# Performance work log

Hardware: AMD Instinct MI355X
Metric: run time of the kernel (lower is better)

The kernel has to match this reference:

```python
import jax, jax.numpy as jnp
import numpy as np

B, P, O, C = 64, 8732, 32, 81
IMG = 224.0
THRESH = 0.5
NEG_POS = 3.0
ALPHA = 1.0


def cxcy_to_xy(b):
    return jnp.concatenate([b[..., :2] - b[..., 2:] / 2, b[..., :2] + b[..., 2:] / 2], -1)


def xy_to_cxcy(b):
    return jnp.concatenate([(b[..., :2] + b[..., 2:]) / 2, b[..., 2:] - b[..., :2]], -1)


def coco_to_xy(b):  # [x, y, w, h] -> [xmin, ymin, xmax, ymax]
    return jnp.concatenate([b[..., :2], b[..., :2] + b[..., 2:]], -1)


def cxcy_to_gcxgcy(cxcy, priors):  # SSD offset encoding, variances 10 / 5
    g_cxcy = (cxcy[..., :2] - priors[..., :2]) / (priors[..., 2:] / 10.0)
    g_wh = jnp.log(cxcy[..., 2:] / priors[..., 2:]) * 5.0
    return jnp.concatenate([g_cxcy, g_wh], -1)


def pairwise_iou(a, b):  # a: [O,4] xy, b: [P,4] xy -> [O,P]
    lt = jnp.maximum(a[:, None, :2], b[None, :, :2])
    rb = jnp.minimum(a[:, None, 2:], b[None, :, 2:])
    wh = jnp.clip(rb - lt, 0.0)
    inter = wh[..., 0] * wh[..., 1]
    area_a = (a[:, 2] - a[:, 0]) * (a[:, 3] - a[:, 1])
    area_b = (b[:, 2] - b[:, 0]) * (b[:, 3] - b[:, 1])
    return inter / (area_a[:, None] + area_b[None, :] - inter)


def setup_inputs() -> dict:
    key = jax.random.key(0)
    k1, k2, k3, k4, k5, k6, k7 = jax.random.split(key, 7)
    pred_locs = jax.random.normal(k1, (B, P, 4), dtype=jnp.float32)
    pred_scores = jax.random.normal(k2, (B, P, C), dtype=jnp.float32)
    # COCO-format gt boxes [x, y, w, h] in pixel coords, guaranteed inside image
    xy = jax.random.uniform(k3, (B, O, 2), minval=0.0, maxval=IMG * 0.55)
    wh = jax.random.uniform(k4, (B, O, 2), minval=8.0, maxval=IMG * 0.4)
    gt_boxes = jnp.concatenate([xy, wh], -1)
    gt_labels = jax.random.randint(k5, (B, O), 1, C)  # foreground labels 1..C-1
    p_cxcy = jax.random.uniform(k6, (P, 2), minval=0.05, maxval=0.95)
    p_wh = jax.random.uniform(k7, (P, 2), minval=0.05, maxval=0.5)
    priors_cxcy = jnp.concatenate([p_cxcy, p_wh], -1)
    return {"pred_locs": pred_locs, "pred_scores": pred_scores,
            "gt_boxes": gt_boxes, "gt_labels": gt_labels,
            "priors_cxcy": priors_cxcy}


def reference(pred_locs, pred_scores, gt_boxes, gt_labels, priors_cxcy):
    priors_xy = cxcy_to_xy(priors_cxcy)

    def match(boxes_coco, labels):  # one image: [O,4] coco, [O] int
        boxes_xy = coco_to_xy(boxes_coco) / IMG  # normalize to [0,1]
        ov = pairwise_iou(boxes_xy, priors_xy)  # [O, P]
        overlap_for_prior = ov.max(axis=0)       # [P]
        object_for_prior = ov.argmax(axis=0)     # [P]
        prior_for_object = ov.argmax(axis=1)     # [O]
        # force each object to claim its best prior
        object_for_prior = object_for_prior.at[prior_for_object].set(jnp.arange(O))
        overlap_for_prior = overlap_for_prior.at[prior_for_object].set(1.0)
        label_for_prior = labels[object_for_prior]
        label_for_prior = jnp.where(overlap_for_prior < THRESH, 0, label_for_prior)
        true_locs = cxcy_to_gcxgcy(xy_to_cxcy(boxes_xy[object_for_prior]), priors_cxcy)
        return true_locs, label_for_prior

    true_locs, true_classes = jax.vmap(match)(gt_boxes, gt_labels)  # [B,P,4], [B,P]

    positive = true_classes != 0          # [B, P]
    n_pos = positive.sum(axis=1)          # [B]
    n_pos_cl = jnp.maximum(n_pos, 1).astype(jnp.float32)
    n_hard_neg = NEG_POS * n_pos_cl

    # SmoothL1 (beta=1), mean over positive prior coords
    diff = jnp.abs(pred_locs - true_locs)
    sl1 = jnp.where(diff < 1.0, 0.5 * diff * diff, diff - 0.5)  # [B,P,4]
    total_pos = n_pos.sum()
    loc_loss = jnp.where(
        total_pos > 0,
        jnp.where(positive[..., None], sl1, 0.0).sum()
        / jnp.maximum(total_pos * 4, 1).astype(jnp.float32),
        0.0,
    )

    # per-prior cross entropy
    logp = jax.nn.log_softmax(pred_scores, axis=-1)
    ce = -jnp.take_along_axis(logp, true_classes[..., None], axis=-1)[..., 0]  # [B,P]

    conf_pos_sum = jnp.where(positive, ce, 0.0).sum()
    ce_neg = jnp.where(positive, 0.0, ce)
    ce_neg_sorted = -jnp.sort(-ce_neg, axis=1)  # descending per image
    ranks = jnp.arange(P)[None, :]
    hard = ranks < n_hard_neg[:, None]
    conf_hard_neg_sum = jnp.where(hard, ce_neg_sorted, 0.0).sum()

    conf_loss = (conf_hard_neg_sum + conf_pos_sum) / n_pos_cl.sum()
    return conf_loss + ALPHA * loc_loss
```

## Files before the change

kernel.cpp:

```cpp
#include <hip/hip_runtime.h>
#include <cstdint>
#include <cstddef>

#define BB 64
#define PP 8732
#define OO 32
#define CC 81
#define NBM 35
#define NB2 273

__global__ __launch_bounds__(256) void k_match(
    const float* __restrict__ gt_boxes,
    const float4* __restrict__ priors,
    float* __restrict__ ovl, int* __restrict__ obj,
    unsigned long long* __restrict__ part)
{
    int b = blockIdx.y, blk = blockIdx.x;
    int tid = threadIdx.x;
    int p = blk * 256 + tid;
    bool pv = p < PP;
    __shared__ float bx1[OO], by1[OO], bx2[OO], by2[OO], bar[OO];
    __shared__ float mat[OO][264];
    __shared__ unsigned long long po[OO][8];
    if (tid < OO) {
        const float* g = gt_boxes + ((size_t)b * OO + tid) * 4;
        float x1 = g[0] / 224.0f, y1 = g[1] / 224.0f;
        float x2 = (g[0] + g[2]) / 224.0f, y2 = (g[1] + g[3]) / 224.0f;
        bx1[tid] = x1; by1[tid] = y1; bx2[tid] = x2; by2[tid] = y2;
        bar[tid] = (x2 - x1) * (y2 - y1);
    }
    __syncthreads();
    float4 pr = priors[pv ? p : 0];
    float px1 = pr.x - pr.z * 0.5f, py1 = pr.y - pr.w * 0.5f;
    float px2 = pr.x + pr.z * 0.5f, py2 = pr.y + pr.w * 0.5f;
    float parea = (px2 - px1) * (py2 - py1);
    float best = -1.0f; int bo = 0;
    #pragma unroll
    for (int o = 0; o < OO; ++o) {
        float lx = fmaxf(bx1[o], px1), ly = fmaxf(by1[o], py1);
        float rx = fminf(bx2[o], px2), ry = fminf(by2[o], py2);
        float w = fmaxf(rx - lx, 0.0f), h = fmaxf(ry - ly, 0.0f);
        float inter = w * h;
        float iou = inter / (bar[o] + parea - inter);
        iou = pv ? iou : 0.0f;
        mat[o][tid] = iou;
        if (iou > best) { best = iou; bo = o; }
    }
    if (pv) {
        size_t idx = (size_t)b * PP + p;
        ovl[idx] = best;
        obj[idx] = bo;
    }
    __syncthreads();
    {
        int o = tid >> 3, j = tid & 7;
        float bv = -1.0f; int bt = 0;
        #pragma unroll
        for (int k = 0; k < 32; ++k) {
            int t = j + 8 * k;
            float v = mat[o][t];
            if (v > bv) { bv = v; bt = t; }
        }
        unsigned pg = (unsigned)(blk * 256 + bt);
        po[o][j] = ((unsigned long long)__float_as_uint(bv) << 32)
                 | (unsigned long long)(0xFFFFFFFFu - pg);
    }
    __syncthreads();
    if (tid < OO) {
        unsigned long long m = po[tid][0];
        #pragma unroll
        for (int j = 1; j < 8; ++j) if (po[tid][j] > m) m = po[tid][j];
        part[((size_t)b * NBM + blk) * OO + tid] = m;
    }
}

__global__ void k_force(const unsigned long long* __restrict__ part,
                        float* __restrict__ ovl, int* __restrict__ obj)
{
    int b = blockIdx.x;
    __shared__ int s_pfo[OO];
    int t = threadIdx.x;
    if (t < OO) {
        unsigned long long m = part[((size_t)b * NBM + 0) * OO + t];
        for (int blk = 1; blk < NBM; ++blk) {
            unsigned long long v = part[((size_t)b * NBM + blk) * OO + t];
            if (v > m) m = v;
        }
        s_pfo[t] = (int)(0xFFFFFFFFu - (unsigned)(m & 0xFFFFFFFFull));
    }
    __syncthreads();
    if (t == 0) {
        for (int o = 0; o < OO; ++o) {
            int p = s_pfo[o];
            obj[(size_t)b * PP + p] = o;
            ovl[(size_t)b * PP + p] = 1.0f;
        }
    }
}

__global__ __launch_bounds__(256) void k_ce(
    const float* __restrict__ scores,
    const float4* __restrict__ pred_locs,
    const float* __restrict__ gt_boxes,
    const int* __restrict__ gt_labels,
    const float4* __restrict__ priors,
    const float* __restrict__ ovl, const int* __restrict__ obj,
    float* __restrict__ ceneg,
    float* __restrict__ pp_posce, float* __restrict__ pp_sl1,
    int* __restrict__ pp_np)
{
    int b = blockIdx.y;
    int group = threadIdx.x >> 4, lane = threadIdx.x & 15;
    int p0 = blockIdx.x * 32 + group;
    int p1 = p0 + 16;
    bool v0 = p0 < PP, v1 = p1 < PP;
    size_t i0 = (size_t)b * PP + (size_t)(v0 ? p0 : 0);
    size_t i1 = (size_t)b * PP + (size_t)(v1 ? p1 : 0);
    __shared__ float s_posce, s_sl1;
    __shared__ int s_np;
    if (threadIdx.x == 0) { s_posce = 0.f; s_sl1 = 0.f; s_np = 0; }
    __syncthreads();
    int lab0 = 0, ob0 = 0, lab1 = 0, ob1 = 0;
    if (v0) { float ov = ovl[i0]; ob0 = obj[i0]; lab0 = (ov < 0.5f) ? 0 : gt_labels[b * OO + ob0]; }
    if (v1) { float ov = ovl[i1]; ob1 = obj[i1]; lab1 = (ov < 0.5f) ? 0 : gt_labels[b * OO + ob1]; }
    const float* r0 = scores + i0 * CC;
    const float* r1 = scores + i1 * CC;
    float a0[6], a1[6];
    #pragma unroll
    for (int k = 0; k < 6; ++k) {
        int c = lane + 16 * k;
        bool cv = c < CC;
        a0[k] = (v0 && cv) ? r0[c] : -INFINITY;
        a1[k] = (v1 && cv) ? r1[c] : -INFINITY;
    }
    float se0 = 0.f, xl0 = 0.f, se1 = 0.f, xl1 = 0.f;
    #pragma unroll
    for (int k = 0; k < 6; ++k) {
        int c = lane + 16 * k;
        if (c < CC) {
            se0 += __expf(a0[k]); if (c == lab0) xl0 = a0[k];
            se1 += __expf(a1[k]); if (c == lab1) xl1 = a1[k];
        }
    }
    #pragma unroll
    for (int s = 8; s >= 1; s >>= 1) {
        se0 += __shfl_xor(se0, s, 16);
        xl0 += __shfl_xor(xl0, s, 16);
        se1 += __shfl_xor(se1, s, 16);
        xl1 += __shfl_xor(xl1, s, 16);
    }
    if (lane == 0) {
        #pragma unroll
        for (int pass = 0; pass < 2; ++pass) {
            bool vv = pass ? v1 : v0;
            if (!vv) continue;
            size_t idx = pass ? i1 : i0;
            int lab = pass ? lab1 : lab0;
            int ob  = pass ? ob1 : ob0;
            int p   = pass ? p1 : p0;
            float se = pass ? se1 : se0;
            float xl = pass ? xl1 : xl0;
            float ce = fmaxf(__logf(se) - xl, 0.0f);
            float cn = ce;
            if (lab != 0) {
                cn = 0.f;
                float4 pl = pred_locs[idx];
                float4 pq = priors[p];
                const float* g = gt_boxes + ((size_t)b * OO + ob) * 4;
                float x1 = g[0] / 224.0f, y1 = g[1] / 224.0f;
                float x2 = (g[0] + g[2]) / 224.0f, y2 = (g[1] + g[3]) / 224.0f;
                float cx = (x1 + x2) * 0.5f, cy = (y1 + y2) * 0.5f;
                float w = x2 - x1, h = y2 - y1;
                float tx = (cx - pq.x) / (pq.z / 10.0f);
                float ty = (cy - pq.y) / (pq.w / 10.0f);
                float tw = __logf(w / pq.z) * 5.0f;
                float th = __logf(h / pq.w) * 5.0f;
                float d0 = fabsf(pl.x - tx), d1 = fabsf(pl.y - ty);
                float d2 = fabsf(pl.z - tw), d3 = fabsf(pl.w - th);
                float sl = (d0 < 1.f ? 0.5f * d0 * d0 : d0 - 0.5f)
                         + (d1 < 1.f ? 0.5f * d1 * d1 : d1 - 0.5f)
                         + (d2 < 1.f ? 0.5f * d2 * d2 : d2 - 0.5f)
                         + (d3 < 1.f ? 0.5f * d3 * d3 : d3 - 0.5f);
                atomicAdd(&s_posce, ce);
                atomicAdd(&s_sl1, sl);
                atomicAdd(&s_np, 1);
            }
            ceneg[idx] = cn;
        }
    }
    __syncthreads();
    if (threadIdx.x == 0) {
        int slot = b * NB2 + blockIdx.x;
        pp_posce[slot] = s_posce;
        pp_sl1[slot]   = s_sl1;
        pp_np[slot]    = s_np;
    }
}

__global__ __launch_bounds__(512) void k_topk(
    const float* __restrict__ ceneg,
    const float* __restrict__ pp_posce, const float* __restrict__ pp_sl1,
    const int* __restrict__ pp_np,
    float* __restrict__ hard, float* __restrict__ posce_b,
    float* __restrict__ sl1_b, int* __restrict__ n_pos)
{
    int b = blockIdx.x, tid = threadIdx.x;
    __shared__ float4 sv4[PP / 4];
    __shared__ int s_i[8];
    __shared__ float s_f[8], s_f2[8];
    __shared__ int s_bcast;
    float pc = 0.f, sl = 0.f; int np = 0;
    for (int i = tid; i < NB2; i += 512) {
        pc += pp_posce[b * NB2 + i];
        sl += pp_sl1[b * NB2 + i];
        np += pp_np[b * NB2 + i];
    }
    #pragma unroll
    for (int s = 32; s >= 1; s >>= 1) {
        pc += __shfl_xor(pc, s, 64);
        sl += __shfl_xor(sl, s, 64);
        np += __shfl_xor(np, s, 64);
    }
    int wid = tid >> 6;
    if ((tid & 63) == 0) { s_i[wid] = np; s_f[wid] = pc; s_f2[wid] = sl; }
    const float4* src = (const float4*)(ceneg + (size_t)b * PP);
    for (int i = tid; i < PP / 4; i += 512) sv4[i] = src[i];
    __syncthreads();
    if (tid == 0) {
        int n = 0; float fp = 0.f, fs = 0.f;
        #pragma unroll
        for (int k = 0; k < 8; ++k) { n += s_i[k]; fp += s_f[k]; fs += s_f2[k]; }
        n_pos[b] = n; posce_b[b] = fp; sl1_b[b] = fs;
        s_bcast = n;
    }
    __syncthreads();
    np = s_bcast;
    int K = 3 * (np > 1 ? np : 1);
    if (K > PP) K = PP;
    unsigned lo = 0u, hi = 0x7F800000u;
    while (hi - lo > 1u) {
        unsigned mid = (lo + hi) >> 1;
        float t = __uint_as_float(mid);
        int c = 0;
        for (int i = tid; i < PP / 4; i += 512) {
            float4 q = sv4[i];
            c += (q.x >= t) + (q.y >= t) + (q.z >= t) + (q.w >= t);
        }
        #pragma unroll
        for (int s = 32; s >= 1; s >>= 1) c += __shfl_xor(c, s, 64);
        if ((tid & 63) == 0) s_i[wid] = c;
        __syncthreads();
        if (tid == 0) {
            int n = 0;
            #pragma unroll
            for (int k = 0; k < 8; ++k) n += s_i[k];
            s_bcast = n;
        }
        __syncthreads();
        int cnt = s_bcast;
        if (cnt >= K) lo = mid; else hi = mid;
        __syncthreads();
    }
    float vk = __uint_as_float(lo);
    float sm = 0.f; int cg = 0;
    for (int i = tid; i < PP / 4; i += 512) {
        float4 q = sv4[i];
        if (q.x > vk) { sm += q.x; cg++; }
        if (q.y > vk) { sm += q.y; cg++; }
        if (q.z > vk) { sm += q.z; cg++; }
        if (q.w > vk) { sm += q.w; cg++; }
    }
    #pragma unroll
    for (int s = 32; s >= 1; s >>= 1) {
        sm += __shfl_xor(sm, s, 64);
        cg += __shfl_xor(cg, s, 64);
    }
    if ((tid & 63) == 0) { s_f[wid] = sm; s_i[wid] = cg; }
    __syncthreads();
    if (tid == 0) {
        float S = 0.f; int CG = 0;
        #pragma unroll
        for (int k = 0; k < 8; ++k) { S += s_f[k]; CG += s_i[k]; }
        hard[b] = S + (float)(K - CG) * vk;
    }
}

__global__ void k_final(const int* __restrict__ n_pos, const float* __restrict__ hard,
                        const float* __restrict__ posce_b, const float* __restrict__ sl1_b,
                        float* __restrict__ out)
{
    int t = threadIdx.x;
    int np = (t < BB) ? n_pos[t] : 0;
    float h  = (t < BB) ? hard[t] : 0.f;
    float pc = (t < BB) ? posce_b[t] : 0.f;
    float sl = (t < BB) ? sl1_b[t] : 0.f;
    float cl = (t < BB) ? (float)(np > 1 ? np : 1) : 0.f;
    int tp = np; float hs = h; float cls = cl;
    #pragma unroll
    for (int s = 32; s >= 1; s >>= 1) {
        tp  += __shfl_xor(tp, s, 64);
        hs  += __shfl_xor(hs, s, 64);
        cls += __shfl_xor(cls, s, 64);
        pc  += __shfl_xor(pc, s, 64);
        sl  += __shfl_xor(sl, s, 64);
    }
    if (t == 0) {
        float conf = (hs + pc) / cls;
        float loc = 0.f;
        if (tp > 0) {
            int den = tp * 4; if (den < 1) den = 1;
            loc = sl / (float)den;
        }
        out[0] = conf + loc;
    }
}

extern "C" void kernel_launch(void* const* d_in, const int* in_sizes, int n_in,
                              void* d_out, int out_size, void* d_ws, size_t ws_size,
                              hipStream_t stream)
{
    const float* pred_locs   = (const float*)d_in[0];
    const float* pred_scores = (const float*)d_in[1];
    const float* gt_boxes    = (const float*)d_in[2];
    const int*   gt_labels   = (const int*)d_in[3];
    const float* priors      = (const float*)d_in[4];

    char* ws = (char*)d_ws;
    const size_t npf = (size_t)BB * PP;
    size_t off = 0;
    float* ovl   = (float*)(ws + off); off += 4 * npf;
    int*   obj   = (int*)  (ws + off); off += 4 * npf;
    float* ceneg = (float*)(ws + off); off += 4 * npf;
    unsigned long long* part = (unsigned long long*)(ws + off); off += 8 * (size_t)BB * NBM * OO;
    float* pp_posce = (float*)(ws + off); off += 4 * (size_t)BB * NB2;
    float* pp_sl1   = (float*)(ws + off); off += 4 * (size_t)BB * NB2;
    int*   pp_np    = (int*)  (ws + off); off += 4 * (size_t)BB * NB2;
    float* posce_b  = (float*)(ws + off); off += 4 * BB;
    float* sl1_b    = (float*)(ws + off); off += 4 * BB;
    int*   n_pos    = (int*)  (ws + off); off += 4 * BB;
    float* hard     = (float*)(ws + off); off += 4 * BB;

    dim3 gM(NBM, BB);
    k_match<<<gM, 256, 0, stream>>>(gt_boxes, (const float4*)priors, ovl, obj, part);

    k_force<<<BB, 64, 0, stream>>>(part, ovl, obj);

    dim3 gB(NB2, BB);
    k_ce<<<gB, 256, 0, stream>>>(pred_scores, (const float4*)pred_locs, gt_boxes, gt_labels,
                                 (const float4*)priors, ovl, obj, ceneg,
                                 pp_posce, pp_sl1, pp_np);

    k_topk<<<BB, 512, 0, stream>>>(ceneg, pp_posce, pp_sl1, pp_np,
                                   hard, posce_b, sl1_b, n_pos);

    k_final<<<1, 64, 0, stream>>>(n_pos, hard, posce_b, sl1_b, (float*)d_out);
}
```

Baseline: 314.5 us.

## Split CE into match-independent logsumexp pass and per-prior label gather

Moves the softmax logsumexp over the score tensor into a new kernel that runs before matching. It stages 64-row tiles in shared memory with coalesced float4 loads and stores per-prior lse and background logit. A second lightweight kernel then gathers the labelled logit per prior and computes the localization loss with one thread per prior, with fewer partial blocks. This removes the dependence of the big streaming pass on matching and improves load coalescing. The cost is an extra launch and two more per-prior workspace arrays.

```diff
diff --git a/kernel.cpp b/kernel.cpp
--- a/kernel.cpp
+++ b/kernel.cpp
@@ -7,7 +7,8 @@
 #define OO 32
 #define CC 81
 #define NBM 35
-#define NB2 273
+#define NBG 35
+#define TR 64
 
 __global__ __launch_bounds__(256) void k_match(
     const float* __restrict__ gt_boxes,
@@ -98,99 +99,98 @@
     }
 }
 
-__global__ __launch_bounds__(256) void k_ce(
+__global__ __launch_bounds__(256) void k_lse(
+    const float* __restrict__ scores,
+    float* __restrict__ lse, float* __restrict__ xbg)
+{
+    int b = blockIdx.y;
+    int p0 = blockIdx.x * TR;
+    int nrows = PP - p0; if (nrows > TR) nrows = TR;
+    int n4 = nrows * CC / 4;
+    __shared__ float4 sv4[TR * CC / 4];
+    const float4* src = (const float4*)(scores + ((size_t)b * PP + p0) * CC);
+    for (int i = threadIdx.x; i < n4; i += 256) sv4[i] = src[i];
+    __syncthreads();
+    const float* sv = (const float*)sv4;
+    int g = threadIdx.x >> 4, l = threadIdx.x & 15;
+    #pragma unroll
+    for (int rr = 0; rr < 4; ++rr) {
+        int r = g * 4 + rr;
+        if (r >= nrows) break;
+        const float* row = sv + r * CC;
+        float se = 0.f;
+        #pragma unroll
+        for (int k = 0; k < 6; ++k) {
+            int c = l + 16 * k;
+            if (c < CC) se += __expf(row[c]);
+        }
+        #pragma unroll
+        for (int s = 8; s >= 1; s >>= 1) se += __shfl_xor(se, s, 16);
+        if (l == 0) {
+            size_t idx = (size_t)b * PP + p0 + r;
+            lse[idx] = __logf(se);
+            xbg[idx] = row[0];
+        }
+    }
+}
+
+__global__ __launch_bounds__(256) void k_gather(
     const float* __restrict__ scores,
     const float4* __restrict__ pred_locs,
     const float* __restrict__ gt_boxes,
     const int* __restrict__ gt_labels,
     const float4* __restrict__ priors,
     const float* __restrict__ ovl, const int* __restrict__ obj,
+    const float* __restrict__ lse, const float* __restrict__ xbg,
     float* __restrict__ ceneg,
     float* __restrict__ pp_posce, float* __restrict__ pp_sl1,
     int* __restrict__ pp_np)
 {
     int b = blockIdx.y;
-    int group = threadIdx.x >> 4, lane = threadIdx.x & 15;
-    int p0 = blockIdx.x * 32 + group;
-    int p1 = p0 + 16;
-    bool v0 = p0 < PP, v1 = p1 < PP;
-    size_t i0 = (size_t)b * PP + (size_t)(v0 ? p0 : 0);
-    size_t i1 = (size_t)b * PP + (size_t)(v1 ? p1 : 0);
+    int p = blockIdx.x * 256 + threadIdx.x;
     __shared__ float s_posce, s_sl1;
     __shared__ int s_np;
     if (threadIdx.x == 0) { s_posce = 0.f; s_sl1 = 0.f; s_np = 0; }
     __syncthreads();
-    int lab0 = 0, ob0 = 0, lab1 = 0, ob1 = 0;
-    if (v0) { float ov = ovl[i0]; ob0 = obj[i0]; lab0 = (ov < 0.5f) ? 0 : gt_labels[b * OO + ob0]; }
-    if (v1) { float ov = ovl[i1]; ob1 = obj[i1]; lab1 = (ov < 0.5f) ? 0 : gt_labels[b * OO + ob1]; }
-    const float* r0 = scores + i0 * CC;
-    const float* r1 = scores + i1 * CC;
-    float a0[6], a1[6];
-    #pragma unroll
-    for (int k = 0; k < 6; ++k) {
-        int c = lane + 16 * k;
-        bool cv = c < CC;
-        a0[k] = (v0 && cv) ? r0[c] : -INFINITY;
-        a1[k] = (v1 && cv) ? r1[c] : -INFINITY;
-    }
-    float se0 = 0.f, xl0 = 0.f, se1 = 0.f, xl1 = 0.f;
-    #pragma unroll
-    for (int k = 0; k < 6; ++k) {
-        int c = lane + 16 * k;
-        if (c < CC) {
-            se0 += __expf(a0[k]); if (c == lab0) xl0 = a0[k];
-            se1 += __expf(a1[k]); if (c == lab1) xl1 = a1[k];
-        }
-    }
-    #pragma unroll
-    for (int s = 8; s >= 1; s >>= 1) {
-        se0 += __shfl_xor(se0, s, 16);
-        xl0 += __shfl_xor(xl0, s, 16);
-        se1 += __shfl_xor(se1, s, 16);
-        xl1 += __shfl_xor(xl1, s, 16);
-    }
-    if (lane == 0) {
-        #pragma unroll
-        for (int pass = 0; pass < 2; ++pass) {
-            bool vv = pass ? v1 : v0;
-            if (!vv) continue;
-            size_t idx = pass ? i1 : i0;
-            int lab = pass ? lab1 : lab0;
-            int ob  = pass ? ob1 : ob0;
-            int p   = pass ? p1 : p0;
-            float se = pass ? se1 : se0;
-            float xl = pass ? xl1 : xl0;
-            float ce = fmaxf(__logf(se) - xl, 0.0f);
-            float cn = ce;
-            if (lab != 0) {
-                cn = 0.f;
-                float4 pl = pred_locs[idx];
-                float4 pq = priors[p];
-                const float* g = gt_boxes + ((size_t)b * OO + ob) * 4;
-                float x1 = g[0] / 224.0f, y1 = g[1] / 224.0f;
-                float x2 = (g[0] + g[2]) / 224.0f, y2 = (g[1] + g[3]) / 224.0f;
-                float cx = (x1 + x2) * 0.5f, cy = (y1 + y2) * 0.5f;
-                float w = x2 - x1, h = y2 - y1;
-                float tx = (cx - pq.x) / (pq.z / 10.0f);
-                float ty = (cy - pq.y) / (pq.w / 10.0f);
-                float tw = __logf(w / pq.z) * 5.0f;
-                float th = __logf(h / pq.w) * 5.0f;
-                float d0 = fabsf(pl.x - tx), d1 = fabsf(pl.y - ty);
-                float d2 = fabsf(pl.z - tw), d3 = fabsf(pl.w - th);
-                float sl = (d0 < 1.f ? 0.5f * d0 * d0 : d0 - 0.5f)
-                         + (d1 < 1.f ? 0.5f * d1 * d1 : d1 - 0.5f)
-                         + (d2 < 1.f ? 0.5f * d2 * d2 : d2 - 0.5f)
-                         + (d3 < 1.f ? 0.5f * d3 * d3 : d3 - 0.5f);
-                atomicAdd(&s_posce, ce);
-                atomicAdd(&s_sl1, sl);
-                atomicAdd(&s_np, 1);
-            }
-            ceneg[idx] = cn;
-        }
+    if (p < PP) {
+        size_t idx = (size_t)b * PP + p;
+        float ov = ovl[idx];
+        int ob = obj[idx];
+        int lab = (ov < 0.5f) ? 0 : gt_labels[b * OO + ob];
+        float L = lse[idx];
+        float cn;
+        if (lab == 0) {
+            cn = fmaxf(L - xbg[idx], 0.0f);
+        } else {
+            float x = scores[idx * CC + lab];
+            float ce = fmaxf(L - x, 0.0f);
+            cn = 0.f;
+            float4 pl = pred_locs[idx];
+            float4 pq = priors[p];
+            const float* g = gt_boxes + ((size_t)b * OO + ob) * 4;
+            float x1 = g[0] / 224.0f, y1 = g[1] / 224.0f;
+            float x2 = (g[0] + g[2]) / 224.0f, y2 = (g[1] + g[3]) / 224.0f;
+            float cx = (x1 + x2) * 0.5f, cy = (y1 + y2) * 0.5f;
+            float w = x2 - x1, h = y2 - y1;
+            float tx = (cx - pq.x) / (pq.z / 10.0f);
+            float ty = (cy - pq.y) / (pq.w / 10.0f);
+            float tw = __logf(w / pq.z) * 5.0f;
+            float th = __logf(h / pq.w) * 5.0f;
+            float d0 = fabsf(pl.x - tx), d1 = fabsf(pl.y - ty);
+            float d2 = fabsf(pl.z - tw), d3 = fabsf(pl.w - th);
+            float sl = (d0 < 1.f ? 0.5f * d0 * d0 : d0 - 0.5f)
+                     + (d1 < 1.f ? 0.5f * d1 * d1 : d1 - 0.5f)
+                     + (d2 < 1.f ? 0.5f * d2 * d2 : d2 - 0.5f)
+                     + (d3 < 1.f ? 0.5f * d3 * d3 : d3 - 0.5f);
+            atomicAdd(&s_posce, ce);
+            atomicAdd(&s_sl1, sl);
+            atomicAdd(&s_np, 1);
+        }
+        ceneg[idx] = cn;
     }
     __syncthreads();
     if (threadIdx.x == 0) {
-        int slot = b * NB2 + blockIdx.x;
+        int slot = b * NBG + blockIdx.x;
         pp_posce[slot] = s_posce;
         pp_sl1[slot]   = s_sl1;
         pp_np[slot]    = s_np;
@@ -210,10 +210,10 @@
     __shared__ float s_f[8], s_f2[8];
     __shared__ int s_bcast;
     float pc = 0.f, sl = 0.f; int np = 0;
-    for (int i = tid; i < NB2; i += 512) {
-        pc += pp_posce[b * NB2 + i];
-        sl += pp_sl1[b * NB2 + i];
-        np += pp_np[b * NB2 + i];
+    for (int i = tid; i < NBG; i += 512) {
+        pc += pp_posce[b * NBG + i];
+        sl += pp_sl1[b * NBG + i];
+        np += pp_np[b * NBG + i];
     }
     #pragma unroll
     for (int s = 32; s >= 1; s >>= 1) {
@@ -331,24 +331,29 @@
     float* ovl   = (float*)(ws + off); off += 4 * npf;
     int*   obj   = (int*)  (ws + off); off += 4 * npf;
     float* ceneg = (float*)(ws + off); off += 4 * npf;
+    float* lse   = (float*)(ws + off); off += 4 * npf;
+    float* xbg   = (float*)(ws + off); off += 4 * npf;
     unsigned long long* part = (unsigned long long*)(ws + off); off += 8 * (size_t)BB * NBM * OO;
-    float* pp_posce = (float*)(ws + off); off += 4 * (size_t)BB * NB2;
-    float* pp_sl1   = (float*)(ws + off); off += 4 * (size_t)BB * NB2;
-    int*   pp_np    = (int*)  (ws + off); off += 4 * (size_t)BB * NB2;
+    float* pp_posce = (float*)(ws + off); off += 4 * (size_t)BB * NBG;
+    float* pp_sl1   = (float*)(ws + off); off += 4 * (size_t)BB * NBG;
+    int*   pp_np    = (int*)  (ws + off); off += 4 * (size_t)BB * NBG;
     float* posce_b  = (float*)(ws + off); off += 4 * BB;
     float* sl1_b    = (float*)(ws + off); off += 4 * BB;
     int*   n_pos    = (int*)  (ws + off); off += 4 * BB;
     float* hard     = (float*)(ws + off); off += 4 * BB;
 
+    dim3 gL((PP + TR - 1) / TR, BB);
+    k_lse<<<gL, 256, 0, stream>>>(pred_scores, lse, xbg);
+
     dim3 gM(NBM, BB);
     k_match<<<gM, 256, 0, stream>>>(gt_boxes, (const float4*)priors, ovl, obj, part);
 
     k_force<<<BB, 64, 0, stream>>>(part, ovl, obj);
 
-    dim3 gB(NB2, BB);
-    k_ce<<<gB, 256, 0, stream>>>(pred_scores, (const float4*)pred_locs, gt_boxes, gt_labels,
-                                 (const float4*)priors, ovl, obj, ceneg,
-                                 pp_posce, pp_sl1, pp_np);
+    dim3 gG(NBG, BB);
+    k_gather<<<gG, 256, 0, stream>>>(pred_scores, (const float4*)pred_locs, gt_boxes,
+                                     gt_labels, (const float4*)priors, ovl, obj,
+                                     lse, xbg, ceneg, pp_posce, pp_sl1, pp_np);
 
     k_topk<<<BB, 512, 0, stream>>>(ceneg, pp_posce, pp_sl1, pp_np,
                                    hard, posce_b, sl1_b, n_pos);
```

Result: slower. 326.7 us (+3.9%).
